# Optimization experiments

Measured on AMD Instinct MI355X. Metric: run time of the kernel, lower is better.

The kernel has to match this reference:

```python
import jax, jax.numpy as jnp
import numpy as np

VOCAB, E, H, OUT = 100000, 300, 300, 5
B, T = 128, 128
PAD = 1


def _uniform(key, shape, stdv):
    return jax.random.uniform(key, shape, jnp.float32, -stdv, stdv)


def setup_inputs() -> dict:
    key = jax.random.key(0)
    ks = jax.random.split(key, 12)
    tokens = jax.random.randint(ks[0], (B, T), 0, VOCAB)
    # valid left-branching transition sequence: S S (R S)*(T-2) R  -> length 2T-1
    tr = np.empty((2 * T - 1,), dtype=np.int32)
    tr[0] = 0; tr[1] = 0
    tr[2:-1:2] = 1; tr[3:-1:2] = 0; tr[-1] = 1
    transitions = jnp.asarray(np.tile(tr[:, None], (1, B)))
    embed_table = jax.random.normal(ks[1], (VOCAB, E), jnp.float32)
    embed_table = embed_table.at[PAD].set(0.0)
    s_e = 1.0 / np.sqrt(E)
    s_h = 1.0 / np.sqrt(H)
    s_2h = 1.0 / np.sqrt(2 * H)
    W_proj = _uniform(ks[2], (E, H), s_e); b_proj = _uniform(ks[3], (H,), s_e)
    W_gate = _uniform(ks[4], (E, H), s_e); b_gate = _uniform(ks[5], (H,), s_e)
    # cell uses reset_parameters with stdv = 1/sqrt(hidden_size)
    W_reduce = _uniform(ks[6], (2 * H, 5 * H), s_h); b_reduce = _uniform(ks[7], (5 * H,), s_h)
    W_out = _uniform(ks[8], (H, OUT), s_h); b_out = _uniform(ks[9], (OUT,), s_h)
    return dict(tokens=tokens, transitions=transitions, embed_table=embed_table,
                W_proj=W_proj, b_proj=b_proj, W_gate=W_gate, b_gate=b_gate,
                W_reduce=W_reduce, b_reduce=b_reduce, W_out=W_out, b_out=b_out)


def _forward(tokens, transitions, embed_table, W_proj, b_proj, W_gate, b_gate,
             W_reduce, b_reduce, W_out, b_out):
    Bn, Tn = tokens.shape
    Hn = W_proj.shape[1]
    # embedding with padding_idx=1 (row zeroed, no grad contribution)
    emb = embed_table[tokens] * (tokens != PAD)[..., None].astype(embed_table.dtype)
    c_buf = emb @ W_proj + b_proj                      # [B,T,H]
    h_buf = jnp.tanh(c_buf) * jax.nn.sigmoid(emb @ W_gate + b_gate)
    buffers = jnp.concatenate([h_buf, c_buf], axis=-1)  # [B,T,2H]

    stack0 = jnp.zeros((Bn, Tn, 2 * Hn), buffers.dtype)
    sp0 = jnp.zeros((Bn,), jnp.int32)                   # stack pointer
    bp0 = jnp.full((Bn,), Tn - 1, jnp.int32)            # buffer pointer (pop from end)
    rows = jnp.arange(Bn)

    def step(carry, tr):
        stack, sp, bp = carry
        # shift candidate: next buffer element
        shift_val = jnp.take_along_axis(buffers, jnp.maximum(bp, 0)[:, None, None], axis=1)[:, 0]
        # reduce candidates: top two of stack (right on top)
        right = jnp.take_along_axis(stack, jnp.maximum(sp - 1, 0)[:, None, None], axis=1)[:, 0]
        left = jnp.take_along_axis(stack, jnp.maximum(sp - 2, 0)[:, None, None], axis=1)[:, 0]
        h_l, c_l = left[:, :Hn], left[:, Hn:]
        h_r, c_r = right[:, :Hn], right[:, Hn:]
        proj = jnp.concatenate([h_l, h_r], axis=-1) @ W_reduce + b_reduce  # [B,5H]
        i, f_l, f_r, g, o = jnp.split(proj, 5, axis=-1)
        c = jax.nn.sigmoid(i) * jnp.tanh(g) + jax.nn.sigmoid(f_l) * c_l + jax.nn.sigmoid(f_r) * c_r
        h = jax.nn.sigmoid(o) * jnp.tanh(c)
        reduced = jnp.concatenate([h, c], axis=-1)       # [B,2H]
        is_shift = (tr == 0)
        new_val = jnp.where(is_shift[:, None], shift_val, reduced)
        pos = jnp.where(is_shift, sp, jnp.maximum(sp - 2, 0))
        stack = stack.at[rows, pos].set(new_val)
        sp = jnp.where(is_shift, sp + 1, sp - 1)
        bp = jnp.where(is_shift, bp - 1, bp)
        return (stack, sp, bp), None

    (stack, sp, bp), _ = jax.lax.scan(step, (stack0, sp0, bp0), transitions)
    root = jnp.take_along_axis(stack, jnp.maximum(sp - 1, 0)[:, None, None], axis=1)[:, 0, :Hn]
    return root @ W_out + b_out                         # [B,OUT] logits


def reference(tokens, transitions, embed_table, W_proj, b_proj, W_gate, b_gate,
              W_reduce, b_reduce, W_out, b_out):
    return _forward(tokens, transitions, embed_table, W_proj, b_proj, W_gate, b_gate,
                    W_reduce, b_reduce, W_out, b_out)
```

## Files before the change

### kernel.cpp

```cpp
#include <hip/hip_runtime.h>

#define VOCAB 100000
#define E 300
#define H 300
#define T 128
#define BB 128
#define NT 255
#define PAD 1
#define NOUT 5

#define RG 8
#define RPB 16
#define CB 30
#define DPB 10
#define COLS 50
#define KP 608
#define KC 8
#define KT 76
#define K4N 19
#define SCAN_THREADS 320
#define MV_THREADS 160
#define CU_THREADS 160
#define SLOTS 32

__device__ __forceinline__ float sigmoidf_(float x) { return 1.0f / (1.0f + expf(-x)); }

__global__ void prep_kernel(const float* __restrict__ Wr, const float* __restrict__ br,
                            float* __restrict__ Wt, float* __restrict__ bpr) {
    int idx = blockIdx.x * 256 + threadIdx.x;
    int total = 1500 * KP;
    if (idx < total) {
        int col = idx / KP, k = idx % KP;
        int cb = col / COLS, rr = col % COLS;
        int g = rr / DPB, jj = rr % DPB;
        int jo = g * 300 + cb * DPB + jj;
        Wt[idx] = (k < 600) ? Wr[k * 1500 + jo] : 0.0f;
        if (k == 0) bpr[col] = br[jo];
    }
}

__global__ void sched_kernel(const int* __restrict__ trans,
                             int* __restrict__ sl, int* __restrict__ sr, int* __restrict__ sd,
                             int* __restrict__ root_tag) {
    __shared__ int stk[64][BB];
    int row = threadIdx.x;
    for (int d = 0; d < 64; ++d) stk[d][row] = -1;
    int sp = 0, bp = T - 1, rid = 0;
    for (int t = 0; t < NT; ++t) {
        int tr = trans[t * BB + row];
        int lt = -1, rt = -1, ds = -1;
        if (tr == 0) {
            int leaf = bp > 0 ? bp : 0;
            if (sp >= 0 && sp < 64) stk[sp][row] = leaf;
            sp += 1; bp -= 1;
        } else {
            int ip = sp - 2 > 0 ? sp - 2 : 0; if (ip > 63) ip = 63;
            int rp = sp - 1 > 0 ? sp - 1 : 0; if (rp > 63) rp = 63;
            lt = stk[ip][row];
            rt = stk[rp][row];
            ds = rid;
            stk[ip][row] = 1000 + rid;
            rid += 1; sp -= 1;
        }
        sl[t * BB + row] = lt; sr[t * BB + row] = rt; sd[t * BB + row] = ds;
    }
    int rp = sp - 1 > 0 ? sp - 1 : 0; if (rp > 63) rp = 63;
    root_tag[row] = stk[rp][row];
}

__global__ void events_kernel(const int* __restrict__ trans,
                              int* __restrict__ ev_t, int* __restrict__ ne) {
    __shared__ int anyf[NT];
    int t = threadIdx.x;
    if (t < NT) {
        const int4* p = (const int4*)(trans + t * BB);
        int o = 0;
        for (int i = 0; i < BB / 4; ++i) { int4 v = p[i]; o |= v.x | v.y | v.z | v.w; }
        anyf[t] = (o != 0) ? 1 : 0;
    }
    __syncthreads();
    if (t == 0) {
        int n = 0;
        for (int i = 0; i < NT; ++i) if (anyf[i]) ev_t[n++] = i;
        *ne = n;
    }
}

__global__ __launch_bounds__(320) void prologue_kernel(
    const int* __restrict__ tokens, const float* __restrict__ embed,
    const float* __restrict__ Wp, const float* __restrict__ bp_,
    const float* __restrict__ Wg, const float* __restrict__ bg_,
    float* __restrict__ hbuf, float* __restrict__ cbuf) {
    __shared__ __align__(16) float As[32][304];
    int m0 = blockIdx.x * 32;
    int tid = threadIdx.x;
    for (int idx = tid; idx < 32 * 300; idx += 320) {
        int r = idx / 300, c = idx % 300;
        int tok = tokens[m0 + r];
        As[r][c] = (tok == PAD) ? 0.0f : embed[(size_t)tok * 300 + c];
    }
    __syncthreads();
    int n = tid;
    if (n < 300) {
        float accP[32], accG[32];
        #pragma unroll
        for (int m = 0; m < 32; ++m) { accP[m] = 0.f; accG[m] = 0.f; }
        #pragma unroll 1
        for (int k4 = 0; k4 < 75; ++k4) {
            int k = k4 * 4;
            float wp0 = Wp[(k + 0) * 300 + n], wp1 = Wp[(k + 1) * 300 + n];
            float wp2 = Wp[(k + 2) * 300 + n], wp3 = Wp[(k + 3) * 300 + n];
            float wg0 = Wg[(k + 0) * 300 + n], wg1 = Wg[(k + 1) * 300 + n];
            float wg2 = Wg[(k + 2) * 300 + n], wg3 = Wg[(k + 3) * 300 + n];
            #pragma unroll
            for (int m = 0; m < 32; ++m) {
                float4 av = *(const float4*)(&As[m][k]);
                accP[m] += av.x * wp0 + av.y * wp1 + av.z * wp2 + av.w * wp3;
                accG[m] += av.x * wg0 + av.y * wg1 + av.z * wg2 + av.w * wg3;
            }
        }
        float bpv = bp_[n], bgv = bg_[n];
        #pragma unroll 1
        for (int m = 0; m < 32; ++m) {
            float c = accP[m] + bpv;
            float g = accG[m] + bgv;
            float h = tanhf(c) * sigmoidf_(g);
            hbuf[(size_t)(m0 + m) * 300 + n] = h;
            cbuf[(size_t)(m0 + m) * 300 + n] = c;
        }
    }
}

struct ScanArgs {
    const int* sl; const int* sr; const int* sd;
    const int* ev_t; const int* ne;
    const float* hbuf; const float* cbuf;
    float* res_h; float* res_c;
    const float* Wt; const float* bpr;
    int* done;
};

__global__ __launch_bounds__(SCAN_THREADS) void scan_kernel(ScanArgs a) {
    __shared__ __align__(16) float xs[RPB][KP];
    __shared__ float sums[COLS][17];
    __shared__ int ltg[RPB], rtg[RPB], dtg[RPB];
    const int tid = threadIdx.x;
    const int bid = blockIdx.x;
    const int rg = bid / CB;
    const int cb = bid % CB;
    const int row0 = rg * RPB;
    const int NEv = *a.ne;

    for (int e = 0; e < NEv; ++e) {
        int t = a.ev_t[e];
        if (tid < RPB) {
            ltg[tid] = a.sl[t * BB + row0 + tid];
            rtg[tid] = a.sr[t * BB + row0 + tid];
            dtg[tid] = a.sd[t * BB + row0 + tid];
        }
        __syncthreads();

        for (int r = 0; r < RPB; ++r) {
            int lt = ltg[r], rt = rtg[r];
            for (int k = tid; k < KP; k += SCAN_THREADS) {
                int tag = (k < 300) ? lt : ((k < 600) ? rt : -1);
                if (tag < 1000) {
                    float v = 0.0f;
                    if (tag >= 0)
                        v = a.hbuf[((size_t)(row0 + r) * T + tag) * H + (k < 300 ? k : k - 300)];
                    xs[r][k] = v;
                }
            }
        }

        if (e > 0 && tid == 0) {
            int guard = 0;
            while (__hip_atomic_load(&a.done[rg * 256 + (e - 1)],
                                     __ATOMIC_RELAXED, __HIP_MEMORY_SCOPE_AGENT) < CB) {
                __builtin_amdgcn_s_sleep(2);
                if (++guard > (1 << 22)) break;
            }
        }
        __syncthreads();

        for (int r = 0; r < RPB; ++r) {
            int lt = ltg[r], rt = rtg[r];
            for (int k = tid; k < 600; k += SCAN_THREADS) {
                int tag = (k < 300) ? lt : rt;
                if (tag >= 1000) {
                    int kk = (k < 300) ? k : (k - 300);
                    const float* src = a.res_h +
                        ((size_t)(row0 + r) * SLOTS + ((tag - 1000) & (SLOTS - 1))) * H + kk;
                    xs[r][k] = __hip_atomic_load((float*)src, __ATOMIC_RELAXED,
                                                 __HIP_MEMORY_SCOPE_AGENT);
                }
            }
        }
        __syncthreads();

        if (tid < MV_THREADS) {
            int kc = tid & 7;
            int rg8 = (tid >> 3) & 1;
            int jg = tid >> 4;
            int r0 = rg8 * 8;
            const float* wbase = a.Wt + ((size_t)(cb * COLS + jg * 5)) * KP + kc * KT;
            float acc[5][8];
            #pragma unroll
            for (int cc = 0; cc < 5; ++cc)
                #pragma unroll
                for (int rr = 0; rr < 8; ++rr) acc[cc][rr] = 0.f;
            #pragma unroll 2
            for (int k4 = 0; k4 < K4N; ++k4) {
                float4 w0 = *(const float4*)(wbase + 0 * KP + k4 * 4);
                float4 w1 = *(const float4*)(wbase + 1 * KP + k4 * 4);
                float4 w2 = *(const float4*)(wbase + 2 * KP + k4 * 4);
                float4 w3 = *(const float4*)(wbase + 3 * KP + k4 * 4);
                float4 w4 = *(const float4*)(wbase + 4 * KP + k4 * 4);
                #pragma unroll
                for (int rr = 0; rr < 8; ++rr) {
                    float4 xv = *(const float4*)(&xs[r0 + rr][kc * KT + k4 * 4]);
                    acc[0][rr] += w0.x * xv.x + w0.y * xv.y + w0.z * xv.z + w0.w * xv.w;
                    acc[1][rr] += w1.x * xv.x + w1.y * xv.y + w1.z * xv.z + w1.w * xv.w;
                    acc[2][rr] += w2.x * xv.x + w2.y * xv.y + w2.z * xv.z + w2.w * xv.w;
                    acc[3][rr] += w3.x * xv.x + w3.y * xv.y + w3.z * xv.z + w3.w * xv.w;
                    acc[4][rr] += w4.x * xv.x + w4.y * xv.y + w4.z * xv.z + w4.w * xv.w;
                }
            }
            #pragma unroll
            for (int d = 1; d < 8; d <<= 1)
                #pragma unroll
                for (int cc = 0; cc < 5; ++cc)
                    #pragma unroll
                    for (int rr = 0; rr < 8; ++rr)
                        acc[cc][rr] += __shfl_xor(acc[cc][rr], d, 64);
            if (kc == 0) {
                #pragma unroll
                for (int cc = 0; cc < 5; ++cc) {
                    float bb = a.bpr[cb * COLS + jg * 5 + cc];
                    #pragma unroll
                    for (int rr = 0; rr < 8; ++rr)
                        sums[jg * 5 + cc][r0 + rr] = acc[cc][rr] + bb;
                }
            }
        }
        __syncthreads();

        if (tid < CU_THREADS) {
            int r = tid & 15, jj = tid >> 4;
            int ds = dtg[r];
            if (ds >= 0) {
                int dim = cb * DPB + jj;
                float iv = sums[jj][r];
                float fl = sums[DPB + jj][r];
                float fr = sums[2 * DPB + jj][r];
                float gv = sums[3 * DPB + jj][r];
                float ov = sums[4 * DPB + jj][r];
                int lt = ltg[r], rt = rtg[r];
                float cl = 0.f, cr = 0.f;
                if (lt >= 0) cl = (lt < 1000)
                    ? a.cbuf[((size_t)(row0 + r) * T + lt) * H + dim]
                    : a.res_c[((size_t)(row0 + r) * SLOTS + ((lt - 1000) & (SLOTS - 1))) * H + dim];
                if (rt >= 0) cr = (rt < 1000)
                    ? a.cbuf[((size_t)(row0 + r) * T + rt) * H + dim]
                    : a.res_c[((size_t)(row0 + r) * SLOTS + ((rt - 1000) & (SLOTS - 1))) * H + dim];
                float c = sigmoidf_(iv) * tanhf(gv) + sigmoidf_(fl) * cl + sigmoidf_(fr) * cr;
                float h = sigmoidf_(ov) * tanhf(c);
                size_t ro = ((size_t)(row0 + r) * SLOTS + (ds & (SLOTS - 1))) * H + dim;
                a.res_c[ro] = c;
                __hip_atomic_store(&a.res_h[ro], h, __ATOMIC_RELAXED,
                                   __HIP_MEMORY_SCOPE_AGENT);
            }
        }
        asm volatile("s_waitcnt vmcnt(0)" ::: "memory");
        __syncthreads();
        if (tid == 0)
            __hip_atomic_fetch_add(&a.done[rg * 256 + e], 1,
                                   __ATOMIC_RELAXED, __HIP_MEMORY_SCOPE_AGENT);
    }
}

__global__ void epilogue_kernel(const int* __restrict__ root_tag,
                                const float* __restrict__ hbuf, const float* __restrict__ res_h,
                                const float* __restrict__ Wo, const float* __restrict__ bo,
                                float* __restrict__ out) {
    int row = blockIdx.x;
    int lane = threadIdx.x;
    int tag = root_tag[row];
    const float* h = nullptr;
    if (tag >= 0)
        h = (tag < 1000) ? hbuf + ((size_t)row * T + tag) * H
                         : res_h + ((size_t)row * SLOTS + ((tag - 1000) & (SLOTS - 1))) * H;
    float acc[NOUT] = {0, 0, 0, 0, 0};
    for (int k = lane; k < H; k += 64) {
        float hv = h ? h[k] : 0.f;
        #pragma unroll
        for (int g = 0; g < NOUT; ++g) acc[g] += hv * Wo[k * NOUT + g];
    }
    #pragma unroll
    for (int d = 1; d < 64; d <<= 1) {
        #pragma unroll
        for (int g = 0; g < NOUT; ++g) acc[g] += __shfl_xor(acc[g], d, 64);
    }
    if (lane == 0) {
        #pragma unroll
        for (int g = 0; g < NOUT; ++g) out[row * NOUT + g] = acc[g] + bo[g];
    }
}

extern "C" void kernel_launch(void* const* d_in, const int* in_sizes, int n_in,
                              void* d_out, int out_size, void* d_ws, size_t ws_size,
                              hipStream_t stream) {
    const int*   tokens = (const int*)d_in[0];
    const int*   trans  = (const int*)d_in[1];
    const float* embed  = (const float*)d_in[2];
    const float* Wp     = (const float*)d_in[3];
    const float* bp     = (const float*)d_in[4];
    const float* Wg     = (const float*)d_in[5];
    const float* bg     = (const float*)d_in[6];
    const float* Wr     = (const float*)d_in[7];
    const float* br     = (const float*)d_in[8];
    const float* Wo     = (const float*)d_in[9];
    const float* bo     = (const float*)d_in[10];
    float* out = (float*)d_out;

    char* ws = (char*)d_ws;
    size_t o = 0;
    auto alloc = [&](size_t bytes) {
        char* p = ws + o;
        o = (o + bytes + 255) & ~(size_t)255;
        return p;
    };
    float* hbuf  = (float*)alloc((size_t)BB * T * H * 4);
    float* cbuf  = (float*)alloc((size_t)BB * T * H * 4);
    float* res_h = (float*)alloc((size_t)BB * SLOTS * H * 4);
    float* res_c = (float*)alloc((size_t)BB * SLOTS * H * 4);
    float* Wt    = (float*)alloc((size_t)1500 * KP * 4);
    float* bpr   = (float*)alloc(1500 * 4);
    int* sl      = (int*)alloc((size_t)NT * BB * 4);
    int* sr      = (int*)alloc((size_t)NT * BB * 4);
    int* sd      = (int*)alloc((size_t)NT * BB * 4);
    int* ev_t    = (int*)alloc(256 * 4);
    int* ne      = (int*)alloc(4);
    int* root    = (int*)alloc(BB * 4);
    int* done    = (int*)alloc(RG * 256 * 4);
    (void)ws_size; (void)in_sizes; (void)n_in; (void)out_size;

    hipMemsetAsync(done, 0, RG * 256 * 4, stream);
    prep_kernel<<<(1500 * KP + 255) / 256, 256, 0, stream>>>(Wr, br, Wt, bpr);
    sched_kernel<<<1, BB, 0, stream>>>(trans, sl, sr, sd, root);
    events_kernel<<<1, 256, 0, stream>>>(trans, ev_t, ne);
    prologue_kernel<<<(BB * T) / 32, 320, 0, stream>>>(tokens, embed, Wp, bp, Wg, bg, hbuf, cbuf);

    ScanArgs sa { sl, sr, sd, ev_t, ne, hbuf, cbuf, res_h, res_c, Wt, bpr, done };
    void* args[] = { &sa };
    hipLaunchCooperativeKernel((const void*)scan_kernel, dim3(RG * CB), dim3(SCAN_THREADS),
                               args, 0, stream);

    epilogue_kernel<<<BB, 64, 0, stream>>>(root, hbuf, res_h, Wo, bo, out);
}
```

Baseline: 3.922 ms.

## Rework scan kernel sync flags, preload schedule, vectorize gathers, split K over 16 lanes

Each block now preloads its full per-event schedule (left, right and destination tags as shorts) into shared memory once, removing per-event global reads. The cross-block barrier changes from one atomic counter per event to per-block flag slots written with plain stores, which a 64-thread wavefront polls in parallel without sleeping. Buffer and result gathers use float4 loads, and the result loads are issued as batched cache-bypassing asm loads. The matvec now uses all 320 threads with a 16-way K split and float2 loads. The per-event flag array is larger, and the spin loop without sleep adds memory traffic while waiting.

```diff
diff --git a/kernel.cpp b/kernel.cpp
--- a/kernel.cpp
+++ b/kernel.cpp
@@ -15,13 +15,12 @@
 #define DPB 10
 #define COLS 50
 #define KP 608
-#define KC 8
-#define KT 76
-#define K4N 19
+#define KC16 16
+#define KT16 38
 #define SCAN_THREADS 320
-#define MV_THREADS 160
 #define CU_THREADS 160
 #define SLOTS 32
+#define EMAX 256
 
 __device__ __forceinline__ float sigmoidf_(float x) { return 1.0f / (1.0f + expf(-x)); }
 
@@ -141,93 +140,122 @@
 };
 
 __global__ __launch_bounds__(SCAN_THREADS) void scan_kernel(ScanArgs a) {
-    __shared__ __align__(16) float xs[RPB][KP];
+    __shared__ __align__(16) float xs[RPB * KP];
     __shared__ float sums[COLS][17];
-    __shared__ int ltg[RPB], rtg[RPB], dtg[RPB];
+    __shared__ int evl[EMAX];
+    __shared__ short sle[EMAX][RPB], sre[EMAX][RPB], sde[EMAX][RPB];
     const int tid = threadIdx.x;
     const int bid = blockIdx.x;
-    const int rg = bid / CB;
-    const int cb = bid % CB;
+    const int rg = bid & 7;
+    const int cb = bid >> 3;
     const int row0 = rg * RPB;
     const int NEv = *a.ne;
 
+    if (tid < EMAX) evl[tid] = (tid < NEv) ? a.ev_t[tid] : 0;
+    __syncthreads();
+    for (int idx = tid; idx < NEv * RPB; idx += SCAN_THREADS) {
+        int e = idx / RPB, r = idx - e * RPB;
+        int t = evl[e];
+        sle[e][r] = (short)a.sl[t * BB + row0 + r];
+        sre[e][r] = (short)a.sr[t * BB + row0 + r];
+        sde[e][r] = (short)a.sd[t * BB + row0 + r];
+    }
+    __syncthreads();
+
     for (int e = 0; e < NEv; ++e) {
-        int t = a.ev_t[e];
-        if (tid < RPB) {
-            ltg[tid] = a.sl[t * BB + row0 + tid];
-            rtg[tid] = a.sr[t * BB + row0 + tid];
-            dtg[tid] = a.sd[t * BB + row0 + tid];
+        #pragma unroll
+        for (int i = 0; i < 8; ++i) {
+            int it = tid + i * SCAN_THREADS;
+            if (it < RPB * (KP / 4)) {
+                int r = it / (KP / 4), q = it - r * (KP / 4);
+                int k = q * 4;
+                int tag = (k < 300) ? (int)sle[e][r] : ((k < 600) ? (int)sre[e][r] : -1);
+                if (tag < 1000) {
+                    float4 v = make_float4(0.f, 0.f, 0.f, 0.f);
+                    if (tag >= 0) {
+                        int kk = (k < 300) ? k : k - 300;
+                        v = *(const float4*)(a.hbuf + ((size_t)(row0 + r) * T + tag) * H + kk);
+                    }
+                    *(float4*)&xs[r * KP + k] = v;
+                }
+            }
+        }
+
+        if (e > 0 && tid < 64) {
+            const int* fp = a.done + (((e - 1) << 3) + rg) * 32 + tid;
+            int guard = 0;
+            bool ok;
+            do {
+                int v = (tid < CB) ? __hip_atomic_load(fp, __ATOMIC_RELAXED,
+                                                       __HIP_MEMORY_SCOPE_AGENT) : 0;
+                ok = (tid < CB) ? (v == e) : true;
+            } while (!__all(ok) && ++guard < (1 << 24));
         }
         __syncthreads();
 
-        for (int r = 0; r < RPB; ++r) {
-            int lt = ltg[r], rt = rtg[r];
-            for (int k = tid; k < KP; k += SCAN_THREADS) {
-                int tag = (k < 300) ? lt : ((k < 600) ? rt : -1);
-                if (tag < 1000) {
-                    float v = 0.0f;
-                    if (tag >= 0)
-                        v = a.hbuf[((size_t)(row0 + r) * T + tag) * H + (k < 300 ? k : k - 300)];
-                    xs[r][k] = v;
-                }
-            }
-        }
-
-        if (e > 0 && tid == 0) {
-            int guard = 0;
-            while (__hip_atomic_load(&a.done[rg * 256 + (e - 1)],
-                                     __ATOMIC_RELAXED, __HIP_MEMORY_SCOPE_AGENT) < CB) {
-                __builtin_amdgcn_s_sleep(2);
-                if (++guard > (1 << 22)) break;
-            }
+        {
+            float4 v0, v1, v2, v3, v4, v5, v6, v7;
+            int w0 = -1, w1 = -1, w2 = -1, w3 = -1, w4 = -1, w5 = -1, w6 = -1, w7 = -1;
+            #define PHB_SLOT(i) { \
+                int it = tid + (i) * SCAN_THREADS; \
+                if (it < 2400) { \
+                    int side = (it >= 1200); int rem = it - (side ? 1200 : 0); \
+                    int r = rem / 75, q = rem - r * 75; \
+                    int tag = side ? (int)sre[e][r] : (int)sle[e][r]; \
+                    if (tag >= 1000) { \
+                        const float* s_ = a.res_h + \
+                            ((size_t)(row0 + r) * SLOTS + ((tag - 1000) & (SLOTS - 1))) * H + q * 4; \
+                        asm volatile("global_load_dwordx4 %0, %1, off sc0 sc1" \
+                                     : "=v"(v##i) : "v"(s_)); \
+                        w##i = r * KP + (side ? 300 : 0) + q * 4; \
+                    } \
+                } }
+            PHB_SLOT(0) PHB_SLOT(1) PHB_SLOT(2) PHB_SLOT(3)
+            PHB_SLOT(4) PHB_SLOT(5) PHB_SLOT(6) PHB_SLOT(7)
+            #undef PHB_SLOT
+            asm volatile("s_waitcnt vmcnt(0)" ::: "memory");
+            if (w0 >= 0) *(float4*)&xs[w0] = v0;
+            if (w1 >= 0) *(float4*)&xs[w1] = v1;
+            if (w2 >= 0) *(float4*)&xs[w2] = v2;
+            if (w3 >= 0) *(float4*)&xs[w3] = v3;
+            if (w4 >= 0) *(float4*)&xs[w4] = v4;
+            if (w5 >= 0) *(float4*)&xs[w5] = v5;
+            if (w6 >= 0) *(float4*)&xs[w6] = v6;
+            if (w7 >= 0) *(float4*)&xs[w7] = v7;
         }
         __syncthreads();
 
-        for (int r = 0; r < RPB; ++r) {
-            int lt = ltg[r], rt = rtg[r];
-            for (int k = tid; k < 600; k += SCAN_THREADS) {
-                int tag = (k < 300) ? lt : rt;
-                if (tag >= 1000) {
-                    int kk = (k < 300) ? k : (k - 300);
-                    const float* src = a.res_h +
-                        ((size_t)(row0 + r) * SLOTS + ((tag - 1000) & (SLOTS - 1))) * H + kk;
-                    xs[r][k] = __hip_atomic_load((float*)src, __ATOMIC_RELAXED,
-                                                 __HIP_MEMORY_SCOPE_AGENT);
-                }
-            }
-        }
-        __syncthreads();
-
-        if (tid < MV_THREADS) {
-            int kc = tid & 7;
-            int rg8 = (tid >> 3) & 1;
-            int jg = tid >> 4;
-            int r0 = rg8 * 8;
-            const float* wbase = a.Wt + ((size_t)(cb * COLS + jg * 5)) * KP + kc * KT;
+        {
+            int kc = tid & 15;
+            int rh = (tid >> 4) & 1;
+            int jg = tid >> 5;
+            int r0 = rh * 8;
+            const float* wb = a.Wt + (size_t)(cb * COLS + jg * 5) * KP + kc * KT16;
+            const float* xb = xs + kc * KT16;
             float acc[5][8];
             #pragma unroll
             for (int cc = 0; cc < 5; ++cc)
                 #pragma unroll
                 for (int rr = 0; rr < 8; ++rr) acc[cc][rr] = 0.f;
-            #pragma unroll 2
-            for (int k4 = 0; k4 < K4N; ++k4) {
-                float4 w0 = *(const float4*)(wbase + 0 * KP + k4 * 4);
-                float4 w1 = *(const float4*)(wbase + 1 * KP + k4 * 4);
-                float4 w2 = *(const float4*)(wbase + 2 * KP + k4 * 4);
-                float4 w3 = *(const float4*)(wbase + 3 * KP + k4 * 4);
-                float4 w4 = *(const float4*)(wbase + 4 * KP + k4 * 4);
+            #pragma unroll 1
+            for (int s = 0; s < KT16 / 2; ++s) {
+                float2 w0 = *(const float2*)(wb + 0 * KP + s * 2);
+                float2 w1 = *(const float2*)(wb + 1 * KP + s * 2);
+                float2 w2 = *(const float2*)(wb + 2 * KP + s * 2);
+                float2 w3 = *(const float2*)(wb + 3 * KP + s * 2);
+                float2 w4 = *(const float2*)(wb + 4 * KP + s * 2);
                 #pragma unroll
                 for (int rr = 0; rr < 8; ++rr) {
-                    float4 xv = *(const float4*)(&xs[r0 + rr][kc * KT + k4 * 4]);
-                    acc[0][rr] += w0.x * xv.x + w0.y * xv.y + w0.z * xv.z + w0.w * xv.w;
-                    acc[1][rr] += w1.x * xv.x + w1.y * xv.y + w1.z * xv.z + w1.w * xv.w;
-                    acc[2][rr] += w2.x * xv.x + w2.y * xv.y + w2.z * xv.z + w2.w * xv.w;
-                    acc[3][rr] += w3.x * xv.x + w3.y * xv.y + w3.z * xv.z + w3.w * xv.w;
-                    acc[4][rr] += w4.x * xv.x + w4.y * xv.y + w4.z * xv.z + w4.w * xv.w;
+                    float2 x = *(const float2*)(xb + (r0 + rr) * KP + s * 2);
+                    acc[0][rr] += w0.x * x.x + w0.y * x.y;
+                    acc[1][rr] += w1.x * x.x + w1.y * x.y;
+                    acc[2][rr] += w2.x * x.x + w2.y * x.y;
+                    acc[3][rr] += w3.x * x.x + w3.y * x.y;
+                    acc[4][rr] += w4.x * x.x + w4.y * x.y;
                 }
             }
             #pragma unroll
-            for (int d = 1; d < 8; d <<= 1)
+            for (int d = 1; d < 16; d <<= 1)
                 #pragma unroll
                 for (int cc = 0; cc < 5; ++cc)
                     #pragma unroll
@@ -247,7 +275,7 @@
 
         if (tid < CU_THREADS) {
             int r = tid & 15, jj = tid >> 4;
-            int ds = dtg[r];
+            int ds = (int)sde[e][r];
             if (ds >= 0) {
                 int dim = cb * DPB + jj;
                 float iv = sums[jj][r];
@@ -255,7 +283,7 @@
                 float fr = sums[2 * DPB + jj][r];
                 float gv = sums[3 * DPB + jj][r];
                 float ov = sums[4 * DPB + jj][r];
-                int lt = ltg[r], rt = rtg[r];
+                int lt = (int)sle[e][r], rt = (int)sre[e][r];
                 float cl = 0.f, cr = 0.f;
                 if (lt >= 0) cl = (lt < 1000)
                     ? a.cbuf[((size_t)(row0 + r) * T + lt) * H + dim]
@@ -274,8 +302,8 @@
         asm volatile("s_waitcnt vmcnt(0)" ::: "memory");
         __syncthreads();
         if (tid == 0)
-            __hip_atomic_fetch_add(&a.done[rg * 256 + e], 1,
-                                   __ATOMIC_RELAXED, __HIP_MEMORY_SCOPE_AGENT);
+            __hip_atomic_store(&a.done[((e << 3) + rg) * 32 + cb], e + 1,
+                               __ATOMIC_RELAXED, __HIP_MEMORY_SCOPE_AGENT);
     }
 }
 
@@ -339,13 +367,13 @@
     int* sl      = (int*)alloc((size_t)NT * BB * 4);
     int* sr      = (int*)alloc((size_t)NT * BB * 4);
     int* sd      = (int*)alloc((size_t)NT * BB * 4);
-    int* ev_t    = (int*)alloc(256 * 4);
+    int* ev_t    = (int*)alloc(EMAX * 4);
     int* ne      = (int*)alloc(4);
     int* root    = (int*)alloc(BB * 4);
-    int* done    = (int*)alloc(RG * 256 * 4);
+    int* done    = (int*)alloc((size_t)EMAX * 8 * 32 * 4);
     (void)ws_size; (void)in_sizes; (void)n_in; (void)out_size;
 
-    hipMemsetAsync(done, 0, RG * 256 * 4, stream);
+    hipMemsetAsync(done, 0, (size_t)EMAX * 8 * 32 * 4, stream);
     prep_kernel<<<(1500 * KP + 255) / 256, 256, 0, stream>>>(Wr, br, Wt, bpr);
     sched_kernel<<<1, BB, 0, stream>>>(trans, sl, sr, sd, root);
     events_kernel<<<1, 256, 0, stream>>>(trans, ev_t, ne);
```

Result: faster. 3.289 ms (-16.1%).
